# Performance work log

Hardware: AMD Instinct MI355X
Metric: run time of the kernel (lower is better)

The kernel has to match this reference:

```python
import jax, jax.numpy as jnp
import numpy as np

D_FIELDS = 16
HIDDEN = 16
N_POINTS = 1_000_000


def setup_inputs() -> dict:
    key = jax.random.key(0)
    ks = jax.random.split(key, 7)
    x = jax.random.normal(ks[0], (1, 3, N_POINTS), dtype=jnp.float32)
    # stacked per-field Conv1d(k=1) weights: conv weight [out,in,1] -> matrix [out,in]
    W1 = jax.random.normal(ks[1], (D_FIELDS, HIDDEN, 3), dtype=jnp.float32) * 0.1
    b1 = jax.random.normal(ks[2], (D_FIELDS, HIDDEN), dtype=jnp.float32) * 0.1
    W2 = jax.random.normal(ks[3], (D_FIELDS, HIDDEN, HIDDEN), dtype=jnp.float32) * 0.1
    b2 = jax.random.normal(ks[4], (D_FIELDS, HIDDEN), dtype=jnp.float32) * 0.1
    W3 = jax.random.normal(ks[5], (D_FIELDS, 3, HIDDEN), dtype=jnp.float32) * 0.1
    b3 = jax.random.normal(ks[6], (D_FIELDS, 3), dtype=jnp.float32) * 0.1
    return {"x": x, "W1": W1, "b1": b1, "W2": W2, "b2": b2, "W3": W3, "b3": b3, "D": D_FIELDS}


def reference(x, W1, b1, W2, b2, W3, b3, D):
    # x: [1, 3, N]. Original loops d in range(D) applying field d's MLP to x and
    # concatenating along dim 0 -> [D, 3, N]. Fused here as batched GEMMs over d.
    xs = x[0]  # [3, N]
    h = jax.nn.relu(jnp.einsum('dhc,cn->dhn', W1, xs) + b1[:, :, None])      # [D,H,N]
    h = jax.nn.relu(jnp.einsum('dgh,dhn->dgn', W2, h) + b2[:, :, None])      # [D,H,N]
    out = jnp.einsum('doh,dhn->don', W3, h) + b3[:, :, None]                 # [D,3,N]
    return out
```

## Files before the change

### kernel.cpp

```cpp
#include <hip/hip_runtime.h>


#define TILES_PER_WAVE 5
#define WAVES_PER_BLOCK 4
#define PTS_PER_BLOCK (TILES_PER_WAVE * WAVES_PER_BLOCK * 16)

typedef __fp16 pk16x2 __attribute__((ext_vector_type(2)));
typedef _Float16 half8_t __attribute__((ext_vector_type(8)));
typedef float float4_t __attribute__((ext_vector_type(4)));

union H2I { pk16x2 h; int i; };
union Frag { half8_t v; int i[4]; };

__device__ __forceinline__ int pkrtz(float a, float b) {
    H2I u; u.h = __builtin_amdgcn_cvt_pkrtz(a, b); return u.i;
}

__global__ __launch_bounds__(256) void fields_mfma_kernel(
    const float* __restrict__ x,
    const float* __restrict__ W1, const float* __restrict__ b1,
    const float* __restrict__ W2, const float* __restrict__ b2,
    const float* __restrict__ W3, const float* __restrict__ b3,
    float* __restrict__ out, int N)
{
    __shared__ __align__(16) _Float16 A1c[16][16][4];
    __shared__ __align__(16) _Float16 A2c[16][16][24];
    __shared__ __align__(16) _Float16 A3c[16][16][24];
    __shared__ __align__(16) float B1c[16][16];
    __shared__ __align__(16) float B2c[16][16];
    __shared__ __align__(16) float B3c[16][16];

    {
        const int td = threadIdx.x;
        const int d = td >> 4, m = td & 15;
        const float* w1 = W1 + (d * 16 + m) * 3;
        A1c[d][m][0] = (_Float16)w1[0];
        A1c[d][m][1] = (_Float16)w1[1];
        A1c[d][m][2] = (_Float16)w1[2];
        A1c[d][m][3] = (_Float16)0.f;
        const float* w2 = W2 + (d * 16 + m) * 16;
#pragma unroll
        for (int k = 0; k < 16; ++k) A2c[d][m][k] = (_Float16)w2[k];
        if (m < 3) {
            const float* w3 = W3 + (d * 3 + m) * 16;
#pragma unroll
            for (int k = 0; k < 16; ++k) A3c[d][m][k] = (_Float16)w3[k];
        } else {
#pragma unroll
            for (int k = 0; k < 16; ++k) A3c[d][m][k] = (_Float16)0.f;
        }
        B1c[d][m] = b1[d * 16 + m];
        B2c[d][m] = b2[d * 16 + m];
        B3c[d][m] = (m < 3) ? b3[d * 3 + m] : 0.f;
    }
    __syncthreads();

    const int lane = threadIdx.x & 63;
    const int wave = threadIdx.x >> 6;
    const int q = lane >> 4;
    const int n16 = lane & 15;

    const int selA = (((n16 + 32 * q) & 63) << 2);
    const int selB = (((n16 + 32 * q + 16) & 63) << 2);

    const int base = blockIdx.x * PTS_PER_BLOCK + wave * (TILES_PER_WAVE * 16);

    Frag xf[TILES_PER_WAVE];
#pragma unroll
    for (int t = 0; t < TILES_PER_WAVE; ++t) {
        const int pt = base + t * 16 + n16;
        float x0 = 0.f, x1 = 0.f, x2 = 0.f;
        if (q == 0 && pt < N) {
            x0 = x[pt];
            x1 = x[(size_t)N + pt];
            x2 = x[2 * (size_t)N + pt];
        }
        xf[t].i[0] = pkrtz(x0, x1);
        xf[t].i[1] = pkrtz(x2, 0.f);
        xf[t].i[2] = 0;
        xf[t].i[3] = 0;
    }

#pragma unroll 1
    for (int d = 0; d < 16; ++d) {
        Frag a1;
        {
            const int* p = (const int*)&A1c[d][n16][0];
            a1.i[0] = (q == 0) ? p[0] : 0;
            a1.i[1] = (q == 0) ? p[1] : 0;
            a1.i[2] = 0; a1.i[3] = 0;
        }
        Frag a2, a3;
        {
            a2.v = *(const half8_t*)&A2c[d][n16][(q & 1) * 8];
            a3.v = *(const half8_t*)&A3c[d][n16][(q & 1) * 8];
            if (q >= 2) { a2.i[0]=0; a2.i[1]=0; a2.i[2]=0; a2.i[3]=0;
                          a3.i[0]=0; a3.i[1]=0; a3.i[2]=0; a3.i[3]=0; }
        }
        const float4_t bias1 = *(const float4_t*)&B1c[d][q * 4];
        const float4_t bias2 = *(const float4_t*)&B2c[d][q * 4];
        const float4_t bias3 = *(const float4_t*)&B3c[d][q * 4];

#pragma unroll
        for (int t = 0; t < TILES_PER_WAVE; ++t) {
            float4_t acc = bias1;
            acc = __builtin_amdgcn_mfma_f32_16x16x32_f16(a1.v, xf[t].v, acc, 0, 0, 0);
            int p0 = pkrtz(fmaxf(acc.x, 0.f), fmaxf(acc.y, 0.f));
            int p1 = pkrtz(fmaxf(acc.z, 0.f), fmaxf(acc.w, 0.f));
            Frag bf;
            bf.i[0] = __builtin_amdgcn_ds_bpermute(selA, p0);
            bf.i[1] = __builtin_amdgcn_ds_bpermute(selA, p1);
            bf.i[2] = __builtin_amdgcn_ds_bpermute(selB, p0);
            bf.i[3] = __builtin_amdgcn_ds_bpermute(selB, p1);
            if (q >= 2) { bf.i[0]=0; bf.i[1]=0; bf.i[2]=0; bf.i[3]=0; }
            acc = bias2;
            acc = __builtin_amdgcn_mfma_f32_16x16x32_f16(a2.v, bf.v, acc, 0, 0, 0);
            p0 = pkrtz(fmaxf(acc.x, 0.f), fmaxf(acc.y, 0.f));
            p1 = pkrtz(fmaxf(acc.z, 0.f), fmaxf(acc.w, 0.f));
            Frag cf;
            cf.i[0] = __builtin_amdgcn_ds_bpermute(selA, p0);
            cf.i[1] = __builtin_amdgcn_ds_bpermute(selA, p1);
            cf.i[2] = __builtin_amdgcn_ds_bpermute(selB, p0);
            cf.i[3] = __builtin_amdgcn_ds_bpermute(selB, p1);
            if (q >= 2) { cf.i[0]=0; cf.i[1]=0; cf.i[2]=0; cf.i[3]=0; }
            acc = bias3;
            acc = __builtin_amdgcn_mfma_f32_16x16x32_f16(a3.v, cf.v, acc, 0, 0, 0);
            const int pt = base + t * 16 + n16;
            if (q == 0 && pt < N) {
                out[(size_t)(d * 3 + 0) * N + pt] = acc.x;
                out[(size_t)(d * 3 + 1) * N + pt] = acc.y;
                out[(size_t)(d * 3 + 2) * N + pt] = acc.z;
            }
        }
    }
}

extern "C" void kernel_launch(void* const* d_in, const int* in_sizes, int n_in,
                              void* d_out, int out_size, void* d_ws, size_t ws_size,
                              hipStream_t stream) {
    const float* x  = (const float*)d_in[0];
    const float* W1 = (const float*)d_in[1];
    const float* b1 = (const float*)d_in[2];
    const float* W2 = (const float*)d_in[3];
    const float* b2 = (const float*)d_in[4];
    const float* W3 = (const float*)d_in[5];
    const float* b3 = (const float*)d_in[6];
    float* out = (float*)d_out;

    const int N = in_sizes[0] / 3;
    const int grid = (N + PTS_PER_BLOCK - 1) / PTS_PER_BLOCK;
    fields_mfma_kernel<<<grid, 256, 0, stream>>>(x, W1, b1, W2, b2, W3, b3, out, N);
}
```

Baseline: 282.1 us.

## Switch to 16x16x16 MFMA so layer outputs feed next layer without permutes

Replaces the 16x16x32 f16 MFMA with the 16x16x16 variant, whose accumulator layout matches the B-operand layout of the next layer. This removes all ds_bpermute shuffles and the zero-masking between layers, and shrinks the LDS weight tables. The K=16 instruction also avoids padding half of each operand with zeros. The kernel may still be bound by output-write bandwidth.

Result: faster. 250.8 us (-11.1%).

```diff
diff --git a/kernel.cpp b/kernel.cpp
--- a/kernel.cpp
+++ b/kernel.cpp
@@ -1,22 +1,24 @@
 #include <hip/hip_runtime.h>
 
+
+#define MFMA16(a, b, c) __builtin_amdgcn_mfma_f32_16x16x16f16((a), (b), (c), 0, 0, 0)
 
 #define TILES_PER_WAVE 5
 #define WAVES_PER_BLOCK 4
 #define PTS_PER_BLOCK (TILES_PER_WAVE * WAVES_PER_BLOCK * 16)
 
 typedef __fp16 pk16x2 __attribute__((ext_vector_type(2)));
-typedef _Float16 half8_t __attribute__((ext_vector_type(8)));
+typedef _Float16 half4_t __attribute__((ext_vector_type(4)));
 typedef float float4_t __attribute__((ext_vector_type(4)));
 
 union H2I { pk16x2 h; int i; };
-union Frag { half8_t v; int i[4]; };
+union Frag { half4_t v; int i[2]; };
 
 __device__ __forceinline__ int pkrtz(float a, float b) {
     H2I u; u.h = __builtin_amdgcn_cvt_pkrtz(a, b); return u.i;
 }
 
-__global__ __launch_bounds__(256) void fields_mfma_kernel(
+__global__ __launch_bounds__(256) void fields_mfma16_kernel(
     const float* __restrict__ x,
     const float* __restrict__ W1, const float* __restrict__ b1,
     const float* __restrict__ W2, const float* __restrict__ b2,
@@ -24,8 +26,8 @@
     float* __restrict__ out, int N)
 {
     __shared__ __align__(16) _Float16 A1c[16][16][4];
-    __shared__ __align__(16) _Float16 A2c[16][16][24];
-    __shared__ __align__(16) _Float16 A3c[16][16][24];
+    __shared__ __align__(16) _Float16 A2c[16][16][16];
+    __shared__ __align__(16) _Float16 A3c[16][16][16];
     __shared__ __align__(16) float B1c[16][16];
     __shared__ __align__(16) float B2c[16][16];
     __shared__ __align__(16) float B3c[16][16];
@@ -60,9 +62,6 @@
     const int q = lane >> 4;
     const int n16 = lane & 15;
 
-    const int selA = (((n16 + 32 * q) & 63) << 2);
-    const int selB = (((n16 + 32 * q + 16) & 63) << 2);
-
     const int base = blockIdx.x * PTS_PER_BLOCK + wave * (TILES_PER_WAVE * 16);
 
     Frag xf[TILES_PER_WAVE];
@@ -77,26 +76,14 @@
         }
         xf[t].i[0] = pkrtz(x0, x1);
         xf[t].i[1] = pkrtz(x2, 0.f);
-        xf[t].i[2] = 0;
-        xf[t].i[3] = 0;
     }
 
 #pragma unroll 1
     for (int d = 0; d < 16; ++d) {
-        Frag a1;
-        {
-            const int* p = (const int*)&A1c[d][n16][0];
-            a1.i[0] = (q == 0) ? p[0] : 0;
-            a1.i[1] = (q == 0) ? p[1] : 0;
-            a1.i[2] = 0; a1.i[3] = 0;
-        }
-        Frag a2, a3;
-        {
-            a2.v = *(const half8_t*)&A2c[d][n16][(q & 1) * 8];
-            a3.v = *(const half8_t*)&A3c[d][n16][(q & 1) * 8];
-            if (q >= 2) { a2.i[0]=0; a2.i[1]=0; a2.i[2]=0; a2.i[3]=0;
-                          a3.i[0]=0; a3.i[1]=0; a3.i[2]=0; a3.i[3]=0; }
-        }
+        Frag a1, a2, a3;
+        a1.v = *(const half4_t*)&A1c[d][n16][0];
+        a2.v = *(const half4_t*)&A2c[d][n16][q * 4];
+        a3.v = *(const half4_t*)&A3c[d][n16][q * 4];
         const float4_t bias1 = *(const float4_t*)&B1c[d][q * 4];
         const float4_t bias2 = *(const float4_t*)&B2c[d][q * 4];
         const float4_t bias3 = *(const float4_t*)&B3c[d][q * 4];
@@ -104,27 +91,17 @@
 #pragma unroll
         for (int t = 0; t < TILES_PER_WAVE; ++t) {
             float4_t acc = bias1;
-            acc = __builtin_amdgcn_mfma_f32_16x16x32_f16(a1.v, xf[t].v, acc, 0, 0, 0);
-            int p0 = pkrtz(fmaxf(acc.x, 0.f), fmaxf(acc.y, 0.f));
-            int p1 = pkrtz(fmaxf(acc.z, 0.f), fmaxf(acc.w, 0.f));
+            acc = MFMA16(a1.v, xf[t].v, acc);
             Frag bf;
-            bf.i[0] = __builtin_amdgcn_ds_bpermute(selA, p0);
-            bf.i[1] = __builtin_amdgcn_ds_bpermute(selA, p1);
-            bf.i[2] = __builtin_amdgcn_ds_bpermute(selB, p0);
-            bf.i[3] = __builtin_amdgcn_ds_bpermute(selB, p1);
-            if (q >= 2) { bf.i[0]=0; bf.i[1]=0; bf.i[2]=0; bf.i[3]=0; }
+            bf.i[0] = pkrtz(fmaxf(acc.x, 0.f), fmaxf(acc.y, 0.f));
+            bf.i[1] = pkrtz(fmaxf(acc.z, 0.f), fmaxf(acc.w, 0.f));
             acc = bias2;
-            acc = __builtin_amdgcn_mfma_f32_16x16x32_f16(a2.v, bf.v, acc, 0, 0, 0);
-            p0 = pkrtz(fmaxf(acc.x, 0.f), fmaxf(acc.y, 0.f));
-            p1 = pkrtz(fmaxf(acc.z, 0.f), fmaxf(acc.w, 0.f));
+            acc = MFMA16(a2.v, bf.v, acc);
             Frag cf;
-            cf.i[0] = __builtin_amdgcn_ds_bpermute(selA, p0);
-            cf.i[1] = __builtin_amdgcn_ds_bpermute(selA, p1);
-            cf.i[2] = __builtin_amdgcn_ds_bpermute(selB, p0);
-            cf.i[3] = __builtin_amdgcn_ds_bpermute(selB, p1);
-            if (q >= 2) { cf.i[0]=0; cf.i[1]=0; cf.i[2]=0; cf.i[3]=0; }
+            cf.i[0] = pkrtz(fmaxf(acc.x, 0.f), fmaxf(acc.y, 0.f));
+            cf.i[1] = pkrtz(fmaxf(acc.z, 0.f), fmaxf(acc.w, 0.f));
             acc = bias3;
-            acc = __builtin_amdgcn_mfma_f32_16x16x32_f16(a3.v, cf.v, acc, 0, 0, 0);
+            acc = MFMA16(a3.v, cf.v, acc);
             const int pt = base + t * 16 + n16;
             if (q == 0 && pt < N) {
                 out[(size_t)(d * 3 + 0) * N + pt] = acc.x;
@@ -149,5 +126,5 @@
 
     const int N = in_sizes[0] / 3;
     const int grid = (N + PTS_PER_BLOCK - 1) / PTS_PER_BLOCK;
-    fields_mfma_kernel<<<grid, 256, 0, stream>>>(x, W1, b1, W2, b2, W3, b3, out, N);
+    fields_mfma16_kernel<<<grid, 256, 0, stream>>>(x, W1, b1, W2, b2, W3, b3, out, N);
 }
```
